# Kernel tuning notes

Measured on AMD Instinct MI355X. Metric: run time of the kernel, lower is better.

## Reference

```python
import jax, jax.numpy as jnp
import numpy as np

EPS = 1e-5  # BatchNorm eps

def setup_inputs() -> dict:
    key = jax.random.key(0)
    ks = jax.random.split(key, 16)
    B, N, C = 8, 4096, 192
    H = C * 4  # dim * mlp_ratio
    scale = 0.02
    return {
        "x":  jax.random.normal(ks[0], (B, N, C), dtype=jnp.float32),
        # fc1: Conv1d(C->H, k=1, bias=False) weight squeezed to [H, C]
        "W1": jax.random.normal(ks[1], (H, C), dtype=jnp.float32) * (1.0 / np.sqrt(C)),
        # BatchNorm1d(H) eval-mode params
        "g1": jax.random.uniform(ks[2], (H,), dtype=jnp.float32, minval=0.5, maxval=1.5),
        "b1": jax.random.normal(ks[3], (H,), dtype=jnp.float32) * 0.1,
        "m1": jax.random.normal(ks[4], (H,), dtype=jnp.float32) * 0.1,
        "v1": jax.random.uniform(ks[5], (H,), dtype=jnp.float32, minval=0.5, maxval=1.5),
        # frequency-domain complex per-channel mixing params (full matrices; einsum uses diagonal)
        "r":  jax.random.normal(ks[6], (H, H), dtype=jnp.float32) * scale,
        "i":  jax.random.normal(ks[7], (H, H), dtype=jnp.float32) * scale,
        "rb": jax.random.normal(ks[8], (H,), dtype=jnp.float32) * scale,
        "ib": jax.random.normal(ks[9], (H,), dtype=jnp.float32) * scale,
        # fc2: Conv1d(H->C, k=1, bias=False) weight squeezed to [C, H]
        "W2": jax.random.normal(ks[10], (C, H), dtype=jnp.float32) * (1.0 / np.sqrt(H)),
        "g2": jax.random.uniform(ks[11], (C,), dtype=jnp.float32, minval=0.5, maxval=1.5),
        "b2": jax.random.normal(ks[12], (C,), dtype=jnp.float32) * 0.1,
        "m2": jax.random.normal(ks[13], (C,), dtype=jnp.float32) * 0.1,
        "v2": jax.random.uniform(ks[14], (C,), dtype=jnp.float32, minval=0.5, maxval=1.5),
    }

def _bn(x, g, b, m, v):
    # eval-mode BatchNorm1d applied on channel (last) axis
    return (x - m) * (g / jnp.sqrt(v + EPS)) + b

def reference(x, W1, g1, b1, m1, v1, r, i, rb, ib, W2, g2, b2, m2, v2):
    # fc1: 1x1 conv over channels + BN + ReLU  -> [B, N, H]
    h = jax.nn.relu(_bn(jnp.einsum('bnc,hc->bnh', x, W1), g1, b1, m1, v1))
    # FFT along token axis (ortho norm)
    xf = jnp.fft.fft(h.astype(jnp.complex64), axis=1, norm='ortho')
    # torch.einsum('bnc,cc->bnc') == per-channel scale by diag of the matrix
    xr = jax.nn.relu(jnp.einsum('bnc,cc->bnc', xf.real, r)
                     - jnp.einsum('bnc,cc->bnc', xf.imag, i) + rb)
    xi = jax.nn.relu(jnp.einsum('bnc,cc->bnc', xf.imag, r)
                     + jnp.einsum('bnc,cc->bnc', xf.real, i) + ib)
    h = jnp.fft.ifft(xr + 1j * xi, axis=1, norm='ortho').real.astype(jnp.float32)
    # fc2: 1x1 conv + BN -> [B, N, C]
    y = _bn(jnp.einsum('bnh,ch->bnc', h, W2), g2, b2, m2, v2)
    return y
```

## Files before the change

kernel.cpp:

```cpp
#include <hip/hip_runtime.h>

typedef float f32x4 __attribute__((ext_vector_type(4)));
typedef __bf16 v8bf __attribute__((ext_vector_type(8)));
typedef unsigned int u32x2 __attribute__((ext_vector_type(2)));

#define B_ 8
#define N_ 4096
#define C_ 192
#define H_ 768

__device__ __forceinline__ unsigned short f2bf(float f) {
  unsigned int u = __float_as_uint(f);
  u += 0x7FFFu + ((u >> 16) & 1u);
  return (unsigned short)(u >> 16);
}
__device__ __forceinline__ unsigned int pk2(float lo, float hi) {
  return (unsigned int)f2bf(lo) | ((unsigned int)f2bf(hi) << 16);
}
__device__ __forceinline__ void unpk(unsigned int w, float& a, float& b) {
  a = __uint_as_float(w << 16);
  b = __uint_as_float(w & 0xFFFF0000u);
}

#define LDS_AS(p) ((__attribute__((address_space(3))) unsigned int*)(void*)(p))
__device__ __forceinline__ void gld16(const void* g, void* l) {
  __builtin_amdgcn_global_load_lds((const __attribute__((address_space(1))) unsigned int*)g,
                                   LDS_AS(l), 16, 0, 0);
}
__device__ __forceinline__ unsigned ldsoff(const void* p) {
  return (unsigned)(size_t)((__attribute__((address_space(3))) char*)(void*)p);
}

__global__ __launch_bounds__(256) void cvtk(
    const float* __restrict__ x, const float* __restrict__ w1, const float* __restrict__ w2,
    unsigned short* __restrict__ xb, unsigned short* __restrict__ w1b,
    unsigned short* __restrict__ w2b) {
  int i = blockIdx.x * 256 + threadIdx.x;
  const float* src; unsigned short* dst; int off;
  if (i < 786432)      { src = x;  dst = xb;  off = i; }
  else if (i < 804864) { src = w1; dst = w1b; off = i - 786432; }
  else                 { src = w2; dst = w2b; off = i - 804864; }
  const float4* s4 = reinterpret_cast<const float4*>(src + (size_t)off * 8);
  float4 a = s4[0], b = s4[1];
  uint4 o;
  o.x = pk2(a.x, a.y); o.y = pk2(a.z, a.w);
  o.z = pk2(b.x, b.y); o.w = pk2(b.z, b.w);
  *reinterpret_cast<uint4*>(dst + (size_t)off * 8) = o;
}

__global__ __launch_bounds__(256) void gemm1k(
    const unsigned short* __restrict__ xb, const unsigned short* __restrict__ W1b,
    const float* __restrict__ g1, const float* __restrict__ b1,
    const float* __restrict__ m1, const float* __restrict__ v1,
    unsigned short* __restrict__ hb) {
  __shared__ __align__(16) unsigned short pool[17408];
  unsigned short* As = pool;
  unsigned short* Bs = pool + 8192;
  unsigned short* Ts = pool;
  const int n0 = blockIdx.x << 7, h0 = blockIdx.y << 7, b = blockIdx.z;
  const int tid = threadIdx.x;
  const int l = tid & 63, q = l >> 4, l16 = l & 15;
  const int wv = tid >> 6, wr = wv >> 1, wc = wv & 1;
  f32x4 acc[4][4];
#pragma unroll
  for (int i_ = 0; i_ < 4; ++i_)
#pragma unroll
    for (int j_ = 0; j_ < 4; ++j_) acc[i_][j_] = {0.f, 0.f, 0.f, 0.f};

  for (int kt = 0; kt < 3; ++kt) {
    const int c0 = kt << 6;
#pragma unroll
    for (int p = 0; p < 4; ++p) {
      int s = tid + (p << 8);
      int row = s >> 3, col = (s & 7) << 3;
      gld16(&xb[(size_t)(b * N_ + n0 + row) * C_ + c0 + col], &As[s << 3]);
    }
#pragma unroll
    for (int p = 0; p < 4; ++p) {
      int s = tid + (p << 8);
      int row = s >> 3, col = (s & 7) << 3;
      gld16(&W1b[(size_t)(h0 + row) * C_ + c0 + col], &Bs[s << 3]);
    }
    __syncthreads();
#pragma unroll
    for (int ks = 0; ks < 2; ++ks) {
      v8bf av[4], bv[4];
#pragma unroll
      for (int f = 0; f < 4; ++f)
        av[f] = *reinterpret_cast<const v8bf*>(&As[((wr << 6) + (f << 4) + l16) * 64 + (ks << 5) + (q << 3)]);
#pragma unroll
      for (int f = 0; f < 4; ++f)
        bv[f] = *reinterpret_cast<const v8bf*>(&Bs[((wc << 6) + (f << 4) + l16) * 64 + (ks << 5) + (q << 3)]);
#pragma unroll
      for (int fm = 0; fm < 4; ++fm)
#pragma unroll
        for (int fn = 0; fn < 4; ++fn)
          acc[fm][fn] = __builtin_amdgcn_mfma_f32_16x16x32_bf16(av[fm], bv[fn], acc[fm][fn], 0, 0, 0);
    }
    __syncthreads();
  }
#pragma unroll
  for (int fn = 0; fn < 4; ++fn) {
    int hl = (wc << 6) + (fn << 4) + l16;
    int hh = h0 + hl;
    float s = g1[hh] * rsqrtf(v1[hh] + 1e-5f);
    float bias = b1[hh] - m1[hh] * s;
#pragma unroll
    for (int fm = 0; fm < 4; ++fm) {
      int nl = (wr << 6) + (fm << 4) + (q << 2);
      ushort4 o;
      o.x = f2bf(fmaxf(acc[fm][fn][0] * s + bias, 0.f));
      o.y = f2bf(fmaxf(acc[fm][fn][1] * s + bias, 0.f));
      o.z = f2bf(fmaxf(acc[fm][fn][2] * s + bias, 0.f));
      o.w = f2bf(fmaxf(acc[fm][fn][3] * s + bias, 0.f));
      *reinterpret_cast<ushort4*>(&Ts[hl * 136 + nl]) = o;
    }
  }
  __syncthreads();
  {
    const int rq = tid >> 4, ch = (tid & 15) << 3;
#pragma unroll
    for (int p = 0; p < 8; ++p) {
      int r = (p << 4) + rq;
      uint4 v = *reinterpret_cast<const uint4*>(&Ts[r * 136 + ch]);
      *reinterpret_cast<uint4*>(&hb[((size_t)(b * H_ + h0 + r) << 12) + n0 + ch]) = v;
    }
  }
}

template <bool INV>
__device__ __forceinline__ void dft4(float& ar, float& ai, float& br, float& bi,
                                     float& cr, float& ci, float& dr, float& di) {
  float t0r = ar + cr, t0i = ai + ci;
  float t1r = ar - cr, t1i = ai - ci;
  float t2r = br + dr, t2i = bi + di;
  float t3r = br - dr, t3i = bi - di;
  ar = t0r + t2r; ai = t0i + t2i;
  cr = t0r - t2r; ci = t0i - t2i;
  if (!INV) { br = t1r + t3i; bi = t1i - t3r; dr = t1r - t3i; di = t1i + t3r; }
  else      { br = t1r - t3i; bi = t1i + t3r; dr = t1r + t3i; di = t1i - t3r; }
}
template <bool INV>
__device__ __forceinline__ void twc(float& xr, float& xi, float wr, float wi) {
  float iw = INV ? -wi : wi;
  float nr = xr * wr - xi * iw;
  xi = xr * iw + xi * wr;
  xr = nr;
}
template <bool INV>
__device__ __forceinline__ void fft16(float* xr, float* xi) {
#pragma unroll
  for (int j = 0; j < 4; ++j)
    dft4<INV>(xr[j], xi[j], xr[j + 4], xi[j + 4], xr[j + 8], xi[j + 8], xr[j + 12], xi[j + 12]);
  const float C1 = 0.9238795325112867f, S1 = -0.3826834323650898f;
  const float C2 = 0.7071067811865476f, S2 = -0.7071067811865476f;
  twc<INV>(xr[5], xi[5], C1, S1);
  twc<INV>(xr[6], xi[6], C2, S2);
  twc<INV>(xr[9], xi[9], C2, S2);
  twc<INV>(xr[7], xi[7], -S1, -C1);
  twc<INV>(xr[13], xi[13], -S1, -C1);
  twc<INV>(xr[10], xi[10], 0.f, -1.f);
  twc<INV>(xr[11], xi[11], -C2, S2);
  twc<INV>(xr[14], xi[14], -C2, S2);
  twc<INV>(xr[15], xi[15], -C1, -S1);
  float yr[16], yi[16];
#pragma unroll
  for (int k = 0; k < 4; ++k) {
    float ar = xr[4 * k], ai = xi[4 * k], br = xr[4 * k + 1], bi = xi[4 * k + 1];
    float cr = xr[4 * k + 2], ci = xi[4 * k + 2], dr = xr[4 * k + 3], di = xi[4 * k + 3];
    dft4<INV>(ar, ai, br, bi, cr, ci, dr, di);
    yr[k] = ar; yi[k] = ai; yr[k + 4] = br; yi[k + 4] = bi;
    yr[k + 8] = cr; yi[k + 8] = ci; yr[k + 12] = dr; yi[k + 12] = di;
  }
#pragma unroll
  for (int qq = 0; qq < 16; ++qq) { xr[qq] = yr[qq]; xi[qq] = yi[qq]; }
}
template <bool INV>
__device__ __forceinline__ void twchain(float* xr, float* xi, int j, float invL) {
  float ang = -6.283185307179586f * (float)j * invL;
  if (INV) ang = -ang;
  float s1, c1;
  __sincosf(ang, &s1, &c1);
  float wr = c1, wi = s1;
#pragma unroll
  for (int r2 = 1; r2 < 16; ++r2) {
    float nr = xr[r2] * wr - xi[r2] * wi;
    xi[r2] = xr[r2] * wi + xi[r2] * wr;
    xr[r2] = nr;
    float t2 = wr * c1 - wi * s1;
    wi = wr * s1 + wi * c1;
    wr = t2;
  }
}

__global__ __launch_bounds__(256) void fftmixk(
    unsigned short* __restrict__ hb, const float* __restrict__ Rm,
    const float* __restrict__ Im, const float* __restrict__ rb,
    const float* __restrict__ ib) {
  __shared__ float2 cxs[4352];
  float* ras = reinterpret_cast<float*>(cxs);
  const int h = blockIdx.x, b = blockIdx.y;
  const int t = threadIdx.x;
  unsigned short* sig = hb + ((size_t)(b * H_ + h) << 12);
  {
    const uint4* src = reinterpret_cast<const uint4*>(sig);
    uint4 w0 = src[2 * t], w1 = src[2 * t + 1];
    float* dst = &ras[17 * t];
    unpk(w0.x, dst[0], dst[1]);  unpk(w0.y, dst[2], dst[3]);
    unpk(w0.z, dst[4], dst[5]);  unpk(w0.w, dst[6], dst[7]);
    unpk(w1.x, dst[8], dst[9]);  unpk(w1.y, dst[10], dst[11]);
    unpk(w1.z, dst[12], dst[13]); unpk(w1.w, dst[14], dst[15]);
  }
  __syncthreads();
  float xr[16], xi[16];
#pragma unroll
  for (int s = 0; s < 16; ++s) {
    int p = t + (s << 8);
    xr[s] = ras[p + (p >> 4)];
    xi[s] = 0.f;
  }
  __syncthreads();
  fft16<false>(xr, xi);
  twchain<false>(xr, xi, t, 1.0f / 4096.0f);
#pragma unroll
  for (int s = 0; s < 16; ++s) {
    int p = t + (s << 8);
    cxs[p + (p >> 4)] = make_float2(xr[s], xi[s]);
  }
  __syncthreads();
  const int cpt = t >> 4, d = t & 15;
#pragma unroll
  for (int s = 0; s < 16; ++s) {
    int p = (cpt << 8) + (s << 4) + d;
    float2 v = cxs[p + (p >> 4)];
    xr[s] = v.x; xi[s] = v.y;
  }
  fft16<false>(xr, xi);
  twchain<false>(xr, xi, d, 1.0f / 256.0f);
#pragma unroll
  for (int s = 0; s < 16; ++s) {
    int p = (cpt << 8) + (s << 4) + d;
    cxs[p + (p >> 4)] = make_float2(xr[s], xi[s]);
  }
  __syncthreads();
#pragma unroll
  for (int s = 0; s < 16; ++s) {
    float2 v = cxs[17 * t + s];
    xr[s] = v.x; xi[s] = v.y;
  }
  fft16<false>(xr, xi);
  {
    const float dr = Rm[(size_t)h * (H_ + 1)];
    const float di = Im[(size_t)h * (H_ + 1)];
    const float rbh = rb[h], ibh = ib[h];
#pragma unroll
    for (int s = 0; s < 16; ++s) {
      float fr = xr[s] * 0.015625f, fi = xi[s] * 0.015625f;
      xr[s] = fmaxf(fmaf(dr, fr, fmaf(-di, fi, rbh)), 0.f);
      xi[s] = fmaxf(fmaf(dr, fi, fmaf(di, fr, ibh)), 0.f);
    }
  }
  fft16<true>(xr, xi);
#pragma unroll
  for (int s = 0; s < 16; ++s) cxs[17 * t + s] = make_float2(xr[s], xi[s]);
  __syncthreads();
#pragma unroll
  for (int s = 0; s < 16; ++s) {
    int p = (cpt << 8) + (s << 4) + d;
    float2 v = cxs[p + (p >> 4)];
    xr[s] = v.x; xi[s] = v.y;
  }
  twchain<true>(xr, xi, d, 1.0f / 256.0f);
  fft16<true>(xr, xi);
#pragma unroll
  for (int s = 0; s < 16; ++s) {
    int p = (cpt << 8) + (s << 4) + d;
    cxs[p + (p >> 4)] = make_float2(xr[s], xi[s]);
  }
  __syncthreads();
#pragma unroll
  for (int s = 0; s < 16; ++s) {
    int p = t + (s << 8);
    float2 v = cxs[p + (p >> 4)];
    xr[s] = v.x; xi[s] = v.y;
  }
  __syncthreads();
  twchain<true>(xr, xi, t, 1.0f / 4096.0f);
  fft16<true>(xr, xi);
#pragma unroll
  for (int s = 0; s < 16; ++s) {
    int p = t + (s << 8);
    ras[p + (p >> 4)] = xr[s];
  }
  __syncthreads();
  {
    const float* s0 = &ras[17 * t];
    unsigned int u[8];
#pragma unroll
    for (int e = 0; e < 8; ++e)
      u[e] = pk2(s0[2 * e] * 0.015625f, s0[2 * e + 1] * 0.015625f);
    uint4* dst = reinterpret_cast<uint4*>(sig);
    dst[2 * t] = make_uint4(u[0], u[1], u[2], u[3]);
    dst[2 * t + 1] = make_uint4(u[4], u[5], u[6], u[7]);
  }
}

__global__ __launch_bounds__(256) void gemm2k(
    const unsigned short* __restrict__ hb, const unsigned short* __restrict__ W2b,
    const float* __restrict__ g2, const float* __restrict__ b2,
    const float* __restrict__ m2, const float* __restrict__ v2,
    float* __restrict__ out) {
  __shared__ __align__(16) float poolf[8704];
  unsigned short* Asw = (unsigned short*)poolf;
  unsigned short* Bsh = (unsigned short*)poolf + 4096;
  float* Tn = poolf;
  const int n0 = blockIdx.x << 7, c0 = blockIdx.y << 6, b = blockIdx.z;
  const int tid = threadIdx.x;
  const int l = tid & 63, q = l >> 4, l16 = l & 15;
  const int wv = tid >> 6, wn2 = wv >> 1, wc2 = wv & 1;
  const unsigned bbase = ldsoff(&Bsh[0]);
  f32x4 acc[2][4];
#pragma unroll
  for (int i_ = 0; i_ < 2; ++i_)
#pragma unroll
    for (int j_ = 0; j_ < 4; ++j_) acc[i_][j_] = {0.f, 0.f, 0.f, 0.f};

  for (int kt = 0; kt < 12; ++kt) {
    const int k0 = kt << 6;
#pragma unroll
    for (int p = 0; p < 2; ++p) {
      int s = tid + (p << 8);
      gld16(&W2b[(size_t)(c0 + (s >> 3)) * H_ + k0 + ((s & 7) << 3)], &Asw[s << 3]);
    }
#pragma unroll
    for (int p = 0; p < 4; ++p) {
      int s = tid + (p << 8);
      int k = ((s >> 6) << 2) | ((s >> 1) & 3);
      int n = (((s >> 3) & 7) << 4) | ((s & 1) << 3);
      gld16(&hb[((size_t)(b * H_ + k0 + k) << 12) + n0 + n], &Bsh[s << 3]);
    }
    __syncthreads();
    v8bf afr[2][2];
#pragma unroll
    for (int fm = 0; fm < 2; ++fm)
#pragma unroll
      for (int ks = 0; ks < 2; ++ks)
        afr[fm][ks] = *reinterpret_cast<const v8bf*>(
            &Asw[((wc2 << 5) + (fm << 4) + l16) * 64 + (ks << 5) + (q << 3)]);
    u32x2 tr[4][2][2];
#pragma unroll
    for (int fn = 0; fn < 4; ++fn)
#pragma unroll
      for (int ks = 0; ks < 2; ++ks) {
        int nidx = (wn2 << 2) + fn;
        unsigned a = bbase + (unsigned)((l16 << 3) + (q << 11) + (ks << 13) + (nidx << 7));
        asm volatile("ds_read_b64_tr_b16 %0, %1 offset:0" : "=v"(tr[fn][ks][0]) : "v"(a));
        asm volatile("ds_read_b64_tr_b16 %0, %1 offset:1024" : "=v"(tr[fn][ks][1]) : "v"(a));
      }
    asm volatile("s_waitcnt lgkmcnt(0)" ::: "memory");
    __builtin_amdgcn_sched_barrier(0);
#pragma unroll
    for (int ks = 0; ks < 2; ++ks)
#pragma unroll
      for (int fn = 0; fn < 4; ++fn) {
        union { unsigned int u[4]; v8bf v; } bb;
        bb.u[0] = tr[fn][ks][0].x; bb.u[1] = tr[fn][ks][0].y;
        bb.u[2] = tr[fn][ks][1].x; bb.u[3] = tr[fn][ks][1].y;
#pragma unroll
        for (int fm = 0; fm < 2; ++fm)
          acc[fm][fn] = __builtin_amdgcn_mfma_f32_16x16x32_bf16(afr[fm][ks], bb.v, acc[fm][fn], 0, 0, 0);
      }
    __syncthreads();
  }
#pragma unroll
  for (int fm = 0; fm < 2; ++fm) {
    int cl = (wc2 << 5) + (fm << 4) + (q << 2);
    int c4 = c0 + cl;
    float4 gv = *reinterpret_cast<const float4*>(&g2[c4]);
    float4 vv = *reinterpret_cast<const float4*>(&v2[c4]);
    float4 bv = *reinterpret_cast<const float4*>(&b2[c4]);
    float4 mv = *reinterpret_cast<const float4*>(&m2[c4]);
    float4 sc, bi;
    sc.x = gv.x * rsqrtf(vv.x + 1e-5f); bi.x = bv.x - mv.x * sc.x;
    sc.y = gv.y * rsqrtf(vv.y + 1e-5f); bi.y = bv.y - mv.y * sc.y;
    sc.z = gv.z * rsqrtf(vv.z + 1e-5f); bi.z = bv.z - mv.z * sc.z;
    sc.w = gv.w * rsqrtf(vv.w + 1e-5f); bi.w = bv.w - mv.w * sc.w;
#pragma unroll
    for (int fn = 0; fn < 4; ++fn) {
      int nl = (wn2 << 6) + (fn << 4) + l16;
      float4 o;
      o.x = acc[fm][fn][0] * sc.x + bi.x;
      o.y = acc[fm][fn][1] * sc.y + bi.y;
      o.z = acc[fm][fn][2] * sc.z + bi.z;
      o.w = acc[fm][fn][3] * sc.w + bi.w;
      *reinterpret_cast<float4*>(&Tn[nl * 68 + cl]) = o;
    }
  }
  __syncthreads();
  {
    const int rq = tid >> 4, ch = (tid & 15) << 2;
#pragma unroll
    for (int p = 0; p < 8; ++p) {
      int r = (p << 4) + rq;
      float4 v = *reinterpret_cast<const float4*>(&Tn[r * 68 + ch]);
      *reinterpret_cast<float4*>(&out[(size_t)(b * N_ + n0 + r) * C_ + c0 + ch]) = v;
    }
  }
}

extern "C" void kernel_launch(void* const* d_in, const int* in_sizes, int n_in,
                              void* d_out, int out_size, void* d_ws, size_t ws_size,
                              hipStream_t stream) {
  const float* x  = (const float*)d_in[0];
  const float* W1 = (const float*)d_in[1];
  const float* g1 = (const float*)d_in[2];
  const float* b1 = (const float*)d_in[3];
  const float* m1 = (const float*)d_in[4];
  const float* v1 = (const float*)d_in[5];
  const float* Rm = (const float*)d_in[6];
  const float* Im = (const float*)d_in[7];
  const float* rb = (const float*)d_in[8];
  const float* ib = (const float*)d_in[9];
  const float* W2 = (const float*)d_in[10];
  const float* g2 = (const float*)d_in[11];
  const float* b2 = (const float*)d_in[12];
  const float* m2 = (const float*)d_in[13];
  const float* v2 = (const float*)d_in[14];
  float* out = (float*)d_out;

  unsigned short* hb  = (unsigned short*)d_ws;
  unsigned short* xb  = hb + (size_t)25165824;
  unsigned short* W1b = xb + (size_t)6291456;
  unsigned short* W2b = W1b + (size_t)147456;

  cvtk<<<3216, 256, 0, stream>>>(x, W1, W2, xb, W1b, W2b);
  gemm1k<<<dim3(32, 6, 8), 256, 0, stream>>>(xb, W1b, g1, b1, m1, v1, hb);
  fftmixk<<<dim3(768, 8), 256, 0, stream>>>(hb, Rm, Im, rb, ib);
  gemm2k<<<dim3(32, 3, 8), 256, 0, stream>>>(hb, W2b, g2, b2, m2, v2, out);
}
```

Baseline: 214.8 us.

## Fuse bf16 conversion into GEMMs and use half-length real FFT in mixer

Removes the separate fp32-to-bf16 conversion kernel and instead converts x, W1 and W2 on the fly inside the GEMM tile loads, using padded LDS rows of 72 elements. The FFT/mix kernel now packs the real signal as a 2048-point complex FFT (radix 16x16x8) and recovers the spectrum through even/odd split twiddles, applying the nonlinear mix pairwise on k and N-k before an inverse half-length transform. It processes two channels per block with half the grid. This cuts FFT work and one pass over memory, but register-path conversion replaces the async global-to-LDS loads, and the split/merge arithmetic adds complexity.

```diff
diff --git a/kernel.cpp b/kernel.cpp
--- a/kernel.cpp
+++ b/kernel.cpp
@@ -31,36 +31,20 @@
   return (unsigned)(size_t)((__attribute__((address_space(3))) char*)(void*)p);
 }
 
-__global__ __launch_bounds__(256) void cvtk(
-    const float* __restrict__ x, const float* __restrict__ w1, const float* __restrict__ w2,
-    unsigned short* __restrict__ xb, unsigned short* __restrict__ w1b,
-    unsigned short* __restrict__ w2b) {
-  int i = blockIdx.x * 256 + threadIdx.x;
-  const float* src; unsigned short* dst; int off;
-  if (i < 786432)      { src = x;  dst = xb;  off = i; }
-  else if (i < 804864) { src = w1; dst = w1b; off = i - 786432; }
-  else                 { src = w2; dst = w2b; off = i - 804864; }
-  const float4* s4 = reinterpret_cast<const float4*>(src + (size_t)off * 8);
-  float4 a = s4[0], b = s4[1];
-  uint4 o;
-  o.x = pk2(a.x, a.y); o.y = pk2(a.z, a.w);
-  o.z = pk2(b.x, b.y); o.w = pk2(b.z, b.w);
-  *reinterpret_cast<uint4*>(dst + (size_t)off * 8) = o;
-}
-
 __global__ __launch_bounds__(256) void gemm1k(
-    const unsigned short* __restrict__ xb, const unsigned short* __restrict__ W1b,
+    const float* __restrict__ x, const float* __restrict__ W1,
     const float* __restrict__ g1, const float* __restrict__ b1,
     const float* __restrict__ m1, const float* __restrict__ v1,
     unsigned short* __restrict__ hb) {
-  __shared__ __align__(16) unsigned short pool[17408];
+  __shared__ __align__(16) unsigned short pool[18432];
   unsigned short* As = pool;
-  unsigned short* Bs = pool + 8192;
+  unsigned short* Bs = pool + 9216;
   unsigned short* Ts = pool;
   const int n0 = blockIdx.x << 7, h0 = blockIdx.y << 7, b = blockIdx.z;
   const int tid = threadIdx.x;
   const int l = tid & 63, q = l >> 4, l16 = l & 15;
   const int wv = tid >> 6, wr = wv >> 1, wc = wv & 1;
+  const int srow = tid >> 3, scol = (tid & 7) << 3;
   f32x4 acc[4][4];
 #pragma unroll
   for (int i_ = 0; i_ < 4; ++i_)
@@ -71,15 +55,21 @@
     const int c0 = kt << 6;
 #pragma unroll
     for (int p = 0; p < 4; ++p) {
-      int s = tid + (p << 8);
-      int row = s >> 3, col = (s & 7) << 3;
-      gld16(&xb[(size_t)(b * N_ + n0 + row) * C_ + c0 + col], &As[s << 3]);
-    }
-#pragma unroll
-    for (int p = 0; p < 4; ++p) {
-      int s = tid + (p << 8);
-      int row = s >> 3, col = (s & 7) << 3;
-      gld16(&W1b[(size_t)(h0 + row) * C_ + c0 + col], &Bs[s << 3]);
+      int row = srow + (p << 5);
+      const float4* sa = reinterpret_cast<const float4*>(
+          &x[(size_t)(b * N_ + n0 + row) * C_ + c0 + scol]);
+      float4 a0 = sa[0], a1 = sa[1];
+      uint4 w;
+      w.x = pk2(a0.x, a0.y); w.y = pk2(a0.z, a0.w);
+      w.z = pk2(a1.x, a1.y); w.w = pk2(a1.z, a1.w);
+      *reinterpret_cast<uint4*>(&As[row * 72 + scol]) = w;
+      const float4* sb = reinterpret_cast<const float4*>(
+          &W1[(size_t)(h0 + row) * C_ + c0 + scol]);
+      float4 b0 = sb[0], b1_ = sb[1];
+      uint4 u;
+      u.x = pk2(b0.x, b0.y); u.y = pk2(b0.z, b0.w);
+      u.z = pk2(b1_.x, b1_.y); u.w = pk2(b1_.z, b1_.w);
+      *reinterpret_cast<uint4*>(&Bs[row * 72 + scol]) = u;
     }
     __syncthreads();
 #pragma unroll
@@ -87,10 +77,10 @@
       v8bf av[4], bv[4];
 #pragma unroll
       for (int f = 0; f < 4; ++f)
-        av[f] = *reinterpret_cast<const v8bf*>(&As[((wr << 6) + (f << 4) + l16) * 64 + (ks << 5) + (q << 3)]);
+        av[f] = *reinterpret_cast<const v8bf*>(&As[((wr << 6) + (f << 4) + l16) * 72 + (ks << 5) + (q << 3)]);
 #pragma unroll
       for (int f = 0; f < 4; ++f)
-        bv[f] = *reinterpret_cast<const v8bf*>(&Bs[((wc << 6) + (f << 4) + l16) * 64 + (ks << 5) + (q << 3)]);
+        bv[f] = *reinterpret_cast<const v8bf*>(&Bs[((wc << 6) + (f << 4) + l16) * 72 + (ks << 5) + (q << 3)]);
 #pragma unroll
       for (int fm = 0; fm < 4; ++fm)
 #pragma unroll
@@ -176,6 +166,22 @@
   for (int qq = 0; qq < 16; ++qq) { xr[qq] = yr[qq]; xi[qq] = yi[qq]; }
 }
 template <bool INV>
+__device__ __forceinline__ void fft8(float* xr, float* xi) {
+  float er[4] = {xr[0], xr[2], xr[4], xr[6]}, ei[4] = {xi[0], xi[2], xi[4], xi[6]};
+  float o_r[4] = {xr[1], xr[3], xr[5], xr[7]}, o_i[4] = {xi[1], xi[3], xi[5], xi[7]};
+  dft4<INV>(er[0], ei[0], er[1], ei[1], er[2], ei[2], er[3], ei[3]);
+  dft4<INV>(o_r[0], o_i[0], o_r[1], o_i[1], o_r[2], o_i[2], o_r[3], o_i[3]);
+  const float c = 0.7071067811865476f;
+  twc<INV>(o_r[1], o_i[1], c, -c);
+  twc<INV>(o_r[2], o_i[2], 0.f, -1.f);
+  twc<INV>(o_r[3], o_i[3], -c, -c);
+#pragma unroll
+  for (int k = 0; k < 4; ++k) {
+    xr[k] = er[k] + o_r[k]; xi[k] = ei[k] + o_i[k];
+    xr[k + 4] = er[k] - o_r[k]; xi[k + 4] = ei[k] - o_i[k];
+  }
+}
+template <bool INV>
 __device__ __forceinline__ void twchain(float* xr, float* xi, int j, float invL) {
   float ang = -6.283185307179586f * (float)j * invL;
   if (INV) ang = -ang;
@@ -193,131 +199,173 @@
   }
 }
 
+__device__ __forceinline__ void mixpair(float2 Zk, float2 Zp, float wr, float wi,
+                                        float dr, float di, float rbh, float ibh,
+                                        float2& G1, float2& G2) {
+  const float sc = 0.015625f;
+  float Er = 0.5f * (Zk.x + Zp.x), Ei = 0.5f * (Zk.y - Zp.y);
+  float Or = 0.5f * (Zk.y + Zp.y), Oi = 0.5f * (Zp.x - Zk.x);
+  float WOr = wr * Or - wi * Oi, WOi = wr * Oi + wi * Or;
+  float X1r = Er + WOr, X1i = Ei + WOi;
+  float X2r = Er - WOr, X2i = Ei - WOi;
+  float p1 = dr * X1r * sc, p2 = di * X1i * sc, p3 = dr * X1i * sc, p4 = di * X1r * sc;
+  float y1r = fmaxf(p1 - p2 + rbh, 0.f), y1i = fmaxf(p3 + p4 + ibh, 0.f);
+  float y4r = fmaxf(p1 + p2 + rbh, 0.f), y4i = fmaxf(p4 - p3 + ibh, 0.f);
+  float q1 = dr * X2r * sc, q2 = di * X2i * sc, q3 = dr * X2i * sc, q4 = di * X2r * sc;
+  float y2r = fmaxf(q1 - q2 + rbh, 0.f), y2i = fmaxf(q3 + q4 + ibh, 0.f);
+  float y3r = fmaxf(q1 + q2 + rbh, 0.f), y3i = fmaxf(q4 - q3 + ibh, 0.f);
+  float Hkr = 0.5f * (y1r + y4r), Hki = 0.5f * (y1i - y4i);
+  float H2r = 0.5f * (y2r + y3r), H2i = 0.5f * (y2i - y3i);
+  float Sr = Hkr + H2r, Si = Hki + H2i;
+  float Dr = Hkr - H2r, Di = Hki - H2i;
+  float P = wi * Dr - wr * Di, Q = wr * Dr + wi * Di;
+  G1 = make_float2(Sr + P, Si + Q);
+  G2 = make_float2(Sr - P, Q - Si);
+}
+
+#define PIDX(i) ((i) + ((i) >> 4))
 __global__ __launch_bounds__(256) void fftmixk(
     unsigned short* __restrict__ hb, const float* __restrict__ Rm,
     const float* __restrict__ Im, const float* __restrict__ rb,
     const float* __restrict__ ib) {
   __shared__ float2 cxs[4352];
-  float* ras = reinterpret_cast<float*>(cxs);
-  const int h = blockIdx.x, b = blockIdx.y;
-  const int t = threadIdx.x;
+  const int b = blockIdx.y;
+  const int tid = threadIdx.x;
+  const int ch = tid >> 7, j = tid & 127;
+  const int h = (blockIdx.x << 1) | ch;
+  const int cb = ch * 2176;
   unsigned short* sig = hb + ((size_t)(b * H_ + h) << 12);
-  {
-    const uint4* src = reinterpret_cast<const uint4*>(sig);
-    uint4 w0 = src[2 * t], w1 = src[2 * t + 1];
-    float* dst = &ras[17 * t];
-    unpk(w0.x, dst[0], dst[1]);  unpk(w0.y, dst[2], dst[3]);
-    unpk(w0.z, dst[4], dst[5]);  unpk(w0.w, dst[6], dst[7]);
-    unpk(w1.x, dst[8], dst[9]);  unpk(w1.y, dst[10], dst[11]);
-    unpk(w1.z, dst[12], dst[13]); unpk(w1.w, dst[14], dst[15]);
-  }
-  __syncthreads();
+  const unsigned int* sig32 = reinterpret_cast<const unsigned int*>(sig);
+  unsigned int* o32 = reinterpret_cast<unsigned int*>(sig);
+
   float xr[16], xi[16];
 #pragma unroll
   for (int s = 0; s < 16; ++s) {
-    int p = t + (s << 8);
-    xr[s] = ras[p + (p >> 4)];
-    xi[s] = 0.f;
-  }
-  __syncthreads();
+    unsigned int w = sig32[j + (s << 7)];
+    unpk(w, xr[s], xi[s]);
+  }
   fft16<false>(xr, xi);
-  twchain<false>(xr, xi, t, 1.0f / 4096.0f);
+  twchain<false>(xr, xi, j, 1.0f / 2048.0f);
+#pragma unroll
+  for (int s = 0; s < 16; ++s) cxs[cb + PIDX(j + (s << 7))] = make_float2(xr[s], xi[s]);
+  __syncthreads();
+  const int c2 = j >> 3, j2 = j & 7;
 #pragma unroll
   for (int s = 0; s < 16; ++s) {
-    int p = t + (s << 8);
-    cxs[p + (p >> 4)] = make_float2(xr[s], xi[s]);
-  }
-  __syncthreads();
-  const int cpt = t >> 4, d = t & 15;
-#pragma unroll
-  for (int s = 0; s < 16; ++s) {
-    int p = (cpt << 8) + (s << 4) + d;
-    float2 v = cxs[p + (p >> 4)];
+    float2 v = cxs[cb + PIDX((c2 << 7) + j2 + (s << 3))];
     xr[s] = v.x; xi[s] = v.y;
   }
   fft16<false>(xr, xi);
-  twchain<false>(xr, xi, d, 1.0f / 256.0f);
-#pragma unroll
-  for (int s = 0; s < 16; ++s) {
-    int p = (cpt << 8) + (s << 4) + d;
-    cxs[p + (p >> 4)] = make_float2(xr[s], xi[s]);
-  }
-  __syncthreads();
-#pragma unroll
-  for (int s = 0; s < 16; ++s) {
-    float2 v = cxs[17 * t + s];
-    xr[s] = v.x; xi[s] = v.y;
-  }
-  fft16<false>(xr, xi);
+  twchain<false>(xr, xi, j2, 1.0f / 128.0f);
+#pragma unroll
+  for (int s = 0; s < 16; ++s) cxs[cb + PIDX((c2 << 7) + j2 + (s << 3))] = make_float2(xr[s], xi[s]);
+  __syncthreads();
+#pragma unroll
+  for (int gg = 0; gg < 2; ++gg) {
+    int g = j + (gg << 7);
+#pragma unroll
+    for (int s = 0; s < 8; ++s) {
+      float2 v = cxs[cb + PIDX((g << 3) + s)];
+      xr[(gg << 3) + s] = v.x; xi[(gg << 3) + s] = v.y;
+    }
+  }
+  __syncthreads();
+#pragma unroll
+  for (int gg = 0; gg < 2; ++gg) {
+    int g = j + (gg << 7);
+    fft8<false>(&xr[gg << 3], &xi[gg << 3]);
+    int kb = (g >> 4) + ((g & 15) << 4);
+#pragma unroll
+    for (int s = 0; s < 8; ++s)
+      cxs[cb + PIDX(kb + (s << 8))] = make_float2(xr[(gg << 3) + s], xi[(gg << 3) + s]);
+  }
+  __syncthreads();
   {
     const float dr = Rm[(size_t)h * (H_ + 1)];
     const float di = Im[(size_t)h * (H_ + 1)];
     const float rbh = rb[h], ibh = ib[h];
-#pragma unroll
-    for (int s = 0; s < 16; ++s) {
-      float fr = xr[s] * 0.015625f, fi = xi[s] * 0.015625f;
-      xr[s] = fmaxf(fmaf(dr, fr, fmaf(-di, fi, rbh)), 0.f);
-      xi[s] = fmaxf(fmaf(dr, fi, fmaf(di, fr, ibh)), 0.f);
-    }
-  }
+    float sn, cs;
+    __sincosf(3.14159265358979f * (float)j / 256.0f, &sn, &cs);
+    float wr = cs, wi = -sn;
+    const float WSR = 0.9999988234517019f, WSI = -0.0015339801862847655f;
+#pragma unroll
+    for (int u = 0; u < 8; ++u) {
+      int k = (j << 3) + u;
+      int kp = (2048 - k) & 2047;
+      float2 Zk = cxs[cb + PIDX(k)];
+      float2 Zp = cxs[cb + PIDX(kp)];
+      float2 G1, G2;
+      mixpair(Zk, Zp, wr, wi, dr, di, rbh, ibh, G1, G2);
+      cxs[cb + PIDX(k)] = G1;
+      cxs[cb + PIDX(kp)] = G2;
+      float nwr = wr * WSR - wi * WSI;
+      wi = wr * WSI + wi * WSR;
+      wr = nwr;
+    }
+    if (j == 0) {
+      float2 Zs = cxs[cb + PIDX(1024)];
+      float2 G1, G2;
+      mixpair(Zs, Zs, 0.f, -1.f, dr, di, rbh, ibh, G1, G2);
+      cxs[cb + PIDX(1024)] = G1;
+    }
+  }
+  __syncthreads();
+#pragma unroll
+  for (int gg = 0; gg < 2; ++gg) {
+    int g = j + (gg << 7);
+    int kb = (g >> 4) + ((g & 15) << 4);
+#pragma unroll
+    for (int s = 0; s < 8; ++s) {
+      float2 v = cxs[cb + PIDX(kb + (s << 8))];
+      xr[(gg << 3) + s] = v.x; xi[(gg << 3) + s] = v.y;
+    }
+  }
+  __syncthreads();
+#pragma unroll
+  for (int gg = 0; gg < 2; ++gg) {
+    int g = j + (gg << 7);
+    fft8<true>(&xr[gg << 3], &xi[gg << 3]);
+#pragma unroll
+    for (int s = 0; s < 8; ++s)
+      cxs[cb + PIDX((g << 3) + s)] = make_float2(xr[(gg << 3) + s], xi[(gg << 3) + s]);
+  }
+  __syncthreads();
+#pragma unroll
+  for (int s = 0; s < 16; ++s) {
+    float2 v = cxs[cb + PIDX((c2 << 7) + j2 + (s << 3))];
+    xr[s] = v.x; xi[s] = v.y;
+  }
+  twchain<true>(xr, xi, j2, 1.0f / 128.0f);
   fft16<true>(xr, xi);
 #pragma unroll
-  for (int s = 0; s < 16; ++s) cxs[17 * t + s] = make_float2(xr[s], xi[s]);
+  for (int s = 0; s < 16; ++s) cxs[cb + PIDX((c2 << 7) + j2 + (s << 3))] = make_float2(xr[s], xi[s]);
   __syncthreads();
 #pragma unroll
   for (int s = 0; s < 16; ++s) {
-    int p = (cpt << 8) + (s << 4) + d;
-    float2 v = cxs[p + (p >> 4)];
+    float2 v = cxs[cb + PIDX(j + (s << 7))];
     xr[s] = v.x; xi[s] = v.y;
   }
-  twchain<true>(xr, xi, d, 1.0f / 256.0f);
+  twchain<true>(xr, xi, j, 1.0f / 2048.0f);
   fft16<true>(xr, xi);
 #pragma unroll
-  for (int s = 0; s < 16; ++s) {
-    int p = (cpt << 8) + (s << 4) + d;
-    cxs[p + (p >> 4)] = make_float2(xr[s], xi[s]);
-  }
-  __syncthreads();
-#pragma unroll
-  for (int s = 0; s < 16; ++s) {
-    int p = t + (s << 8);
-    float2 v = cxs[p + (p >> 4)];
-    xr[s] = v.x; xi[s] = v.y;
-  }
-  __syncthreads();
-  twchain<true>(xr, xi, t, 1.0f / 4096.0f);
-  fft16<true>(xr, xi);
-#pragma unroll
-  for (int s = 0; s < 16; ++s) {
-    int p = t + (s << 8);
-    ras[p + (p >> 4)] = xr[s];
-  }
-  __syncthreads();
-  {
-    const float* s0 = &ras[17 * t];
-    unsigned int u[8];
-#pragma unroll
-    for (int e = 0; e < 8; ++e)
-      u[e] = pk2(s0[2 * e] * 0.015625f, s0[2 * e + 1] * 0.015625f);
-    uint4* dst = reinterpret_cast<uint4*>(sig);
-    dst[2 * t] = make_uint4(u[0], u[1], u[2], u[3]);
-    dst[2 * t + 1] = make_uint4(u[4], u[5], u[6], u[7]);
-  }
+  for (int s = 0; s < 16; ++s)
+    o32[j + (s << 7)] = pk2(xr[s] * 0.015625f, xi[s] * 0.015625f);
 }
 
 __global__ __launch_bounds__(256) void gemm2k(
-    const unsigned short* __restrict__ hb, const unsigned short* __restrict__ W2b,
+    const unsigned short* __restrict__ hb, const float* __restrict__ W2,
     const float* __restrict__ g2, const float* __restrict__ b2,
     const float* __restrict__ m2, const float* __restrict__ v2,
     float* __restrict__ out) {
   __shared__ __align__(16) float poolf[8704];
   unsigned short* Asw = (unsigned short*)poolf;
-  unsigned short* Bsh = (unsigned short*)poolf + 4096;
+  unsigned short* Bsh = (unsigned short*)poolf + 4608;
   float* Tn = poolf;
   const int n0 = blockIdx.x << 7, c0 = blockIdx.y << 6, b = blockIdx.z;
   const int tid = threadIdx.x;
   const int l = tid & 63, q = l >> 4, l16 = l & 15;
   const int wv = tid >> 6, wn2 = wv >> 1, wc2 = wv & 1;
+  const int srow = tid >> 3, scol = (tid & 7) << 3;
   const unsigned bbase = ldsoff(&Bsh[0]);
   f32x4 acc[2][4];
 #pragma unroll
@@ -329,8 +377,14 @@
     const int k0 = kt << 6;
 #pragma unroll
     for (int p = 0; p < 2; ++p) {
-      int s = tid + (p << 8);
-      gld16(&W2b[(size_t)(c0 + (s >> 3)) * H_ + k0 + ((s & 7) << 3)], &Asw[s << 3]);
+      int row = srow + (p << 5);
+      const float4* sa = reinterpret_cast<const float4*>(
+          &W2[(size_t)(c0 + row) * H_ + k0 + scol]);
+      float4 a0 = sa[0], a1 = sa[1];
+      uint4 w;
+      w.x = pk2(a0.x, a0.y); w.y = pk2(a0.z, a0.w);
+      w.z = pk2(a1.x, a1.y); w.w = pk2(a1.z, a1.w);
+      *reinterpret_cast<uint4*>(&Asw[row * 72 + scol]) = w;
     }
 #pragma unroll
     for (int p = 0; p < 4; ++p) {
@@ -346,7 +400,7 @@
 #pragma unroll
       for (int ks = 0; ks < 2; ++ks)
         afr[fm][ks] = *reinterpret_cast<const v8bf*>(
-            &Asw[((wc2 << 5) + (fm << 4) + l16) * 64 + (ks << 5) + (q << 3)]);
+            &Asw[((wc2 << 5) + (fm << 4) + l16) * 72 + (ks << 5) + (q << 3)]);
     u32x2 tr[4][2][2];
 #pragma unroll
     for (int fn = 0; fn < 4; ++fn)
@@ -428,13 +482,9 @@
   const float* v2 = (const float*)d_in[14];
   float* out = (float*)d_out;
 
-  unsigned short* hb  = (unsigned short*)d_ws;
-  unsigned short* xb  = hb + (size_t)25165824;
-  unsigned short* W1b = xb + (size_t)6291456;
-  unsigned short* W2b = W1b + (size_t)147456;
-
-  cvtk<<<3216, 256, 0, stream>>>(x, W1, W2, xb, W1b, W2b);
-  gemm1k<<<dim3(32, 6, 8), 256, 0, stream>>>(xb, W1b, g1, b1, m1, v1, hb);
-  fftmixk<<<dim3(768, 8), 256, 0, stream>>>(hb, Rm, Im, rb, ib);
-  gemm2k<<<dim3(32, 3, 8), 256, 0, stream>>>(hb, W2b, g2, b2, m2, v2, out);
-}
+  unsigned short* hb = (unsigned short*)d_ws;
+
+  gemm1k<<<dim3(32, 6, 8), 256, 0, stream>>>(x, W1, g1, b1, m1, v1, hb);
+  fftmixk<<<dim3(384, 8), 256, 0, stream>>>(hb, Rm, Im, rb, ib);
+  gemm2k<<<dim3(32, 3, 8), 256, 0, stream>>>(hb, W2, g2, b2, m2, v2, out);
+}
```

Measured after the change: 203.8 us. 5.1% less time.
